# Kernel tuning notes

Measured on AMD Instinct MI355X. Metric: run time of the kernel, lower is better.

## Reference

```python
import jax, jax.numpy as jnp
import numpy as np

NQ, NK, D = 8192, 8192, 256
NEG_INF = -1e30


def setup_inputs() -> dict:
    key = jax.random.key(0)
    kK, kV, kQ, kM = jax.random.split(key, 4)
    K = jax.random.normal(kK, (NK, D), dtype=jnp.float32)
    V = jax.random.normal(kV, (NK, D), dtype=jnp.float32)
    Q = jax.random.normal(kQ, (NQ, D), dtype=jnp.float32)
    m = jax.random.randint(kM, (NQ, NK), 0, 2) > 0  # bool mask, True = attend
    return {"K": K, "V": V, "Q": Q, "m": m}


def reference(K, V, Q, m):
    # affinity: scaled dot product with optional mask
    scale = 1.0 / jnp.sqrt(jnp.asarray(D, dtype=Q.dtype))
    QKt = jnp.einsum('qd,kd->qk', Q, K) * scale  # [NQ, NK]
    QKt = jnp.where(m, QKt, NEG_INF)
    # normalization: softmax over keys
    QKt_n = jax.nn.softmax(QKt, axis=-1)
    # weighted sum of values
    return QKt_n @ V  # [NQ, D]
```

## Files before the change

kernel.cpp:

```cpp
#include <hip/hip_runtime.h>
#include <stdint.h>
#include <stddef.h>

#define NQS 8192
#define NKS 8192
#define DS  256

typedef _Float16 half8 __attribute__((ext_vector_type(8)));
typedef _Float16 half4v __attribute__((ext_vector_type(4)));
typedef float floatx16 __attribute__((ext_vector_type(16)));
typedef float floatx4e __attribute__((ext_vector_type(4)));
typedef uint32_t uint32x4 __attribute__((ext_vector_type(4)));

#define MFMA32(A,B,C) __builtin_amdgcn_mfma_f32_32x32x16_f16(A,B,C,0,0,0)

#define GLOAD_LDS16(gp, lp) \
  __builtin_amdgcn_global_load_lds((const __attribute__((address_space(1))) void*)(gp), \
                                   (__attribute__((address_space(3))) void*)(lp), 16, 0, 0)

#define TILE_ELEMS 16384
#define SUB_ELEMS  8192

__global__ void detect_mask(const uint4* __restrict__ M, uint32_t* __restrict__ flag){
  __shared__ uint32_t s[256];
  uint32_t acc = 0;
  for (int i = threadIdx.x; i < 4096; i += 256){
    uint4 v = M[i];
    acc |= v.x | v.y | v.z | v.w;
  }
  s[threadIdx.x] = acc;
  __syncthreads();
  if (threadIdx.x == 0){
    uint32_t t = 0;
    for (int i = 0; i < 256; i++) t |= s[i];
    *flag = (t > 1u) ? 1u : 0u;
  }
}

__global__ void prep(const float* __restrict__ Qf, const float* __restrict__ K,
                     const float* __restrict__ V,
                     _Float16* __restrict__ Qh, _Float16* __restrict__ Kc,
                     _Float16* __restrict__ Vc){
  const int tid = threadIdx.x;
  if (blockIdx.x < 1024){
    size_t u = (size_t)blockIdx.x*256 + tid;
    const float4* src = (const float4*)(Qf + u*8);
    float4 a = src[0], b = src[1];
    half8 h = {(_Float16)a.x,(_Float16)a.y,(_Float16)a.z,(_Float16)a.w,
               (_Float16)b.x,(_Float16)b.y,(_Float16)b.z,(_Float16)b.w};
    *(half8*)(Qh + u*8) = h;
  } else if (blockIdx.x < 2048){
    int gid = (blockIdx.x - 1024)*256 + tid;
    int key = gid & 8191;
    int c   = gid >> 13;
    int kt = c >> 1, t = c & 1;
    const float4* s = (const float4*)(K + (size_t)key*DS + kt*16 + t*8);
    float4 x = s[0], y = s[1];
    half8 h = {(_Float16)x.x,(_Float16)x.y,(_Float16)x.z,(_Float16)x.w,
               (_Float16)y.x,(_Float16)y.y,(_Float16)y.z,(_Float16)y.w};
    int tile = key >> 6, mt = (key >> 5) & 1, k32 = key & 31;
    size_t off = (size_t)tile*TILE_ELEMS + (((mt*16 + kt)*2 + t)*32 + k32)*8;
    *(half8*)(Kc + off) = h;
  } else {
    int gid = (blockIdx.x - 2048)*256 + tid;
    int d32 = gid & 31;
    int t   = (gid >> 5) & 1;
    int nt  = (gid >> 6) & 7;
    int kkt = (gid >> 9) & 3;
    int tile = gid >> 11;
    int d = nt*32 + d32;
    int kb8 = tile*64 + kkt*16 + t*8;
    half8 h;
    #pragma unroll
    for (int j=0;j<8;j++) h[j] = (_Float16)V[(size_t)(kb8 + j)*DS + d];
    *(half8*)(Vc + (size_t)gid*8) = h;
  }
}

__global__ __launch_bounds__(256, 2) void attn_fwd(
  const _Float16* __restrict__ Qh, const _Float16* __restrict__ Kc,
  const _Float16* __restrict__ Vc, const uint8_t* __restrict__ Msk,
  const uint32_t* __restrict__ flag, _Float16* __restrict__ Oph,
  float* __restrict__ Lo)
{
  __shared__ _Float16 Kls[2][SUB_ELEMS];
  __shared__ _Float16 Vls[2][SUB_ELEMS];
  __shared__ uint8_t  Pk[16][128][8];

  const int tid  = threadIdx.x;
  const int w    = tid >> 6;
  const int lane = tid & 63;
  const int q32  = lane & 31;
  const int t    = lane >> 5;
  const int b    = blockIdx.x;
  const int kh   = b & 7;
  const int rb   = (b >> 3)*128;
  const int rowbase = rb + w*32;
  const int sub0 = kh << 5;
  const int kbase = kh << 10;

  const float kLog = 0.09016844005556021f;
  const float MFIX = 6.0f;

  const bool bm = (*flag != 0u);

  {
    const size_t base = (size_t)sub0 * SUB_ELEMS;
    #pragma unroll
    for (int j=0;j<4;j++){
      int c = w*4 + j;
      GLOAD_LDS16(Kc + base + c*512 + lane*8, &Kls[0][c*512]);
      GLOAD_LDS16(Vc + base + c*512 + lane*8, &Vls[0][c*512]);
    }
  }

  if (bm){
    const uint8_t* mrow = Msk + (size_t)(rb + (tid>>1))*NKS + kbase + (tid&1)*16;
    #pragma unroll 1
    for (int sp=0; sp<16; ++sp){
      uint32x4 e = __builtin_nontemporal_load((const uint32x4*)(mrow + sp*64));
      uint32x4 o = __builtin_nontemporal_load((const uint32x4*)(mrow + sp*64 + 32));
      #pragma unroll
      for (int q=0;q<4;q++){
        uint32_t xe = e[q], xo = o[q];
        uint8_t ne = (uint8_t)(((xe&0x000000FFu)?1u:0u)|((xe&0x0000FF00u)?2u:0u)|
                               ((xe&0x00FF0000u)?4u:0u)|((xe&0xFF000000u)?8u:0u));
        uint8_t no = (uint8_t)(((xo&0x000000FFu)?1u:0u)|((xo&0x0000FF00u)?2u:0u)|
                               ((xo&0x00FF0000u)?4u:0u)|((xo&0xFF000000u)?8u:0u));
        Pk[sp][tid>>1][(tid&1)*4 + q] = (uint8_t)(ne | (no << 4));
      }
    }
  } else {
    const uint32_t* M32 = (const uint32_t*)Msk;
    #pragma unroll 1
    for (int sp=0; sp<16; ++sp){
      uint32x4 e[4], o[4];
      #pragma unroll
      for (int jj=0;jj<4;jj++){
        const uint32_t* p = M32 + (size_t)(rb + jj*32 + (tid>>3))*NKS + kbase + sp*64 + (tid&7)*4;
        e[jj] = __builtin_nontemporal_load((const uint32x4*)p);
        o[jj] = __builtin_nontemporal_load((const uint32x4*)(p + 32));
      }
      #pragma unroll
      for (int jj=0;jj<4;jj++){
        uint8_t ne = (uint8_t)((e[jj][0]?1u:0u)|(e[jj][1]?2u:0u)|(e[jj][2]?4u:0u)|(e[jj][3]?8u:0u));
        uint8_t no = (uint8_t)((o[jj][0]?1u:0u)|(o[jj][1]?2u:0u)|(o[jj][2]?4u:0u)|(o[jj][3]?8u:0u));
        Pk[sp][jj*32 + (tid>>3)][tid&7] = (uint8_t)(ne | (no << 4));
      }
    }
  }

  half8 qf[16];
  {
    const _Float16* qrow = Qh + (size_t)(rowbase + q32)*DS;
    #pragma unroll
    for (int kt=0;kt<16;kt++)
      qf[kt] = *(const half8*)(qrow + kt*16 + t*8);
  }

  floatx16 O[8];
  #pragma unroll
  for (int nt=0;nt<8;nt++)
    #pragma unroll
    for (int i=0;i<16;i++) O[nt][i] = 0.f;
  float lsum = 0.f;

  __syncthreads();

  #pragma unroll 1
  for (int it=0; it<32; ++it){
    const int buf = it & 1;

    if (it < 31){
      const size_t base = (size_t)(sub0 + it + 1) * SUB_ELEMS;
      #pragma unroll
      for (int j=0;j<4;j++){
        int c = w*4 + j;
        GLOAD_LDS16(Kc + base + c*512 + lane*8, &Kls[buf^1][c*512]);
        GLOAD_LDS16(Vc + base + c*512 + lane*8, &Vls[buf^1][c*512]);
      }
    }

    const uint2 nq = *(const uint2*)&Pk[it>>1][w*32 + q32][0];
    const int sh = (it & 1) * 4;
    const uint32_t nib_s[4] = { (nq.x >> (8*t + sh))      & 0xFu,
                                (nq.x >> (16 + 8*t + sh)) & 0xFu,
                                (nq.y >> (8*t + sh))      & 0xFu,
                                (nq.y >> (16 + 8*t + sh)) & 0xFu };

    floatx16 S0, S1;
    #pragma unroll
    for (int i=0;i<16;i++){ S0[i]=0.f; S1[i]=0.f; }
    #pragma unroll
    for (int kt=0;kt<8;kt++){
      half8 kA = *(const half8*)&Kls[buf][((kt*2 + t)*32 + q32)*8];
      S0 = MFMA32(kA, qf[kt], S0);
    }
    #pragma unroll
    for (int kt=8;kt<16;kt++){
      half8 kA = *(const half8*)&Kls[buf][((kt*2 + t)*32 + q32)*8];
      S1 = MFMA32(kA, qf[kt], S1);
    }

    uint32_t pk[4][2];
    #pragma unroll
    for (int s=0;s<4;s++){
      float pv[4];
      #pragma unroll
      for (int rr=0;rr<4;rr++){
        int i = s*4 + rr;
        float e = __builtin_amdgcn_exp2f(__builtin_fmaf(S0[i]+S1[i], kLog, -MFIX));
        float p = ((nib_s[s] >> rr) & 1u) ? e : 0.f;
        lsum += p;
        pv[rr] = p;
      }
      pk[s][0] = __builtin_bit_cast(uint32_t, __builtin_amdgcn_cvt_pkrtz(pv[0], pv[1]));
      pk[s][1] = __builtin_bit_cast(uint32_t, __builtin_amdgcn_cvt_pkrtz(pv[2], pv[3]));
    }

    #pragma unroll
    for (int kt2=0; kt2<2; ++kt2){
      const int s_own  = kt2*2 + t;
      const int s_send = kt2*2 + (t^1);
      uint32_t r0 = __shfl_xor(__builtin_bit_cast(int, pk[s_send][0]), 32);
      uint32_t r1 = __shfl_xor(__builtin_bit_cast(int, pk[s_send][1]), 32);
      uint32_t lo0 = (t==0) ? pk[s_own][0] : r0;
      uint32_t lo1 = (t==0) ? pk[s_own][1] : r1;
      uint32_t hi0 = (t==0) ? r0 : pk[s_own][0];
      uint32_t hi1 = (t==0) ? r1 : pk[s_own][1];
      uint4 u = {lo0, lo1, hi0, hi1};
      half8 pa = __builtin_bit_cast(half8, u);
      #pragma unroll
      for (int nt=0;nt<8;nt++){
        half8 vB = *(const half8*)&Vls[buf][(((kt2*8+nt)*2 + t)*32 + q32)*8];
        O[nt] = MFMA32(pa, vB, O[nt]);
      }
    }

    __syncthreads();
  }

  lsum += __builtin_bit_cast(float, __shfl_xor(__builtin_bit_cast(int, lsum), 32));
  if (t == 0) __builtin_nontemporal_store(lsum, &Lo[(size_t)b*128 + w*32 + q32]);

  _Float16* ob = Oph + ((size_t)b*128 + w*32)*256;
  #pragma unroll
  for (int nt=0;nt<8;nt++){
    #pragma unroll
    for (int i=0;i<16;i++){
      int row = (i&3) + 8*(i>>2) + 4*t;
      __builtin_nontemporal_store((_Float16)O[nt][i], &ob[(size_t)row*256 + nt*32 + q32]);
    }
  }
}

__global__ void combine8(const _Float16* __restrict__ Oph, const float* __restrict__ Lo,
                         float* __restrict__ Out){
  int gid = blockIdx.x*256 + threadIdx.x;
  int row = gid >> 6;
  int c4  = (gid & 63) << 2;
  int g   = row >> 7, r = row & 127;

  float lt = 0.f;
  #pragma unroll
  for (int kh=0;kh<8;kh++) lt += __builtin_nontemporal_load(&Lo[(size_t)(g*8 + kh)*128 + r]);
  float li = 1.0f / lt;

  floatx4e acc = {0.f,0.f,0.f,0.f};
  #pragma unroll
  for (int kh=0;kh<8;kh++){
    half4v o = __builtin_nontemporal_load(
        (const half4v*)(Oph + ((size_t)(g*8 + kh)*128 + r)*256 + c4));
    acc[0] += (float)o[0]; acc[1] += (float)o[1];
    acc[2] += (float)o[2]; acc[3] += (float)o[3];
  }
  acc[0] *= li; acc[1] *= li; acc[2] *= li; acc[3] *= li;
  __builtin_nontemporal_store(acc, (floatx4e*)(Out + (size_t)row*DS + c4));
}

extern "C" void kernel_launch(void* const* d_in, const int* in_sizes, int n_in,
                              void* d_out, int out_size, void* d_ws, size_t ws_size,
                              hipStream_t stream){
  (void)in_sizes; (void)n_in; (void)out_size; (void)ws_size;
  const float*   K = (const float*)d_in[0];
  const float*   V = (const float*)d_in[1];
  const float*   Q = (const float*)d_in[2];
  const uint8_t* M = (const uint8_t*)d_in[3];
  float* Out = (float*)d_out;

  _Float16* Qh  = (_Float16*)d_ws;
  _Float16* Kc  = Qh + (size_t)NQS*DS;
  _Float16* Vc  = Kc + (size_t)NKS*DS;
  _Float16* Oph = Vc + (size_t)NKS*DS;
  float*    Lo  = (float*)(Oph + (size_t)512*128*256);
  uint32_t* flag = (uint32_t*)(Lo + 512*128);

  hipLaunchKernelGGL(detect_mask, dim3(1),    dim3(256), 0, stream, (const uint4*)M, flag);
  hipLaunchKernelGGL(prep,        dim3(3072), dim3(256), 0, stream, Q, K, V, Qh, Kc, Vc);
  hipLaunchKernelGGL(attn_fwd,    dim3(512),  dim3(256), 0, stream, Qh, Kc, Vc, M, flag, Oph, Lo);
  hipLaunchKernelGGL(combine8,    dim3(2048), dim3(256), 0, stream, Oph, Lo, Out);
}
```

Before: 468.6 us.

## Stream mask packing into the main loop instead of the prologue

In the word-per-element mask path, only the first two mask sub-tiles are packed up front. The remaining sub-tiles are loaded into registers one iteration ahead and packed into the shared bitmask during the main attention loop. This hides the long serial mask-load prologue behind the MFMA work. In exchange it adds register pressure from eight held uint32x4 values and extra branching inside the hot loop.

After: 502.5 us. +7.3%, slower.

```diff
diff --git a/kernel.cpp b/kernel.cpp
--- a/kernel.cpp
+++ b/kernel.cpp
@@ -103,6 +103,9 @@
   const float MFIX = 6.0f;
 
   const bool bm = (*flag != 0u);
+  const uint32_t* M32 = (const uint32_t*)Msk;
+  const uint32_t* mbase32 = M32 + (size_t)(rb + (tid>>3))*NKS + kbase + (tid&7)*4;
+  const size_t mrowstride = (size_t)32*NKS;
 
   {
     const size_t base = (size_t)sub0 * SUB_ELEMS;
@@ -114,7 +117,31 @@
     }
   }
 
-  if (bm){
+  uint32x4 B[8];
+  if (!bm){
+    #pragma unroll
+    for (int sp=0; sp<2; ++sp){
+      uint32x4 e[4], o[4];
+      #pragma unroll
+      for (int jj=0;jj<4;jj++){
+        const uint32_t* p = mbase32 + jj*mrowstride + sp*64;
+        e[jj] = __builtin_nontemporal_load((const uint32x4*)p);
+        o[jj] = __builtin_nontemporal_load((const uint32x4*)(p + 32));
+      }
+      #pragma unroll
+      for (int jj=0;jj<4;jj++){
+        uint8_t ne = (uint8_t)((e[jj][0]?1u:0u)|(e[jj][1]?2u:0u)|(e[jj][2]?4u:0u)|(e[jj][3]?8u:0u));
+        uint8_t no = (uint8_t)((o[jj][0]?1u:0u)|(o[jj][1]?2u:0u)|(o[jj][2]?4u:0u)|(o[jj][3]?8u:0u));
+        Pk[sp][jj*32 + (tid>>3)][tid&7] = (uint8_t)(ne | (no << 4));
+      }
+    }
+    #pragma unroll
+    for (int jj=0;jj<4;jj++){
+      const uint32_t* p = mbase32 + jj*mrowstride + 2*64;
+      B[jj*2]   = __builtin_nontemporal_load((const uint32x4*)p);
+      B[jj*2+1] = __builtin_nontemporal_load((const uint32x4*)(p + 32));
+    }
+  } else {
     const uint8_t* mrow = Msk + (size_t)(rb + (tid>>1))*NKS + kbase + (tid&1)*16;
     #pragma unroll 1
     for (int sp=0; sp<16; ++sp){
@@ -130,24 +157,6 @@
         Pk[sp][tid>>1][(tid&1)*4 + q] = (uint8_t)(ne | (no << 4));
       }
     }
-  } else {
-    const uint32_t* M32 = (const uint32_t*)Msk;
-    #pragma unroll 1
-    for (int sp=0; sp<16; ++sp){
-      uint32x4 e[4], o[4];
-      #pragma unroll
-      for (int jj=0;jj<4;jj++){
-        const uint32_t* p = M32 + (size_t)(rb + jj*32 + (tid>>3))*NKS + kbase + sp*64 + (tid&7)*4;
-        e[jj] = __builtin_nontemporal_load((const uint32x4*)p);
-        o[jj] = __builtin_nontemporal_load((const uint32x4*)(p + 32));
-      }
-      #pragma unroll
-      for (int jj=0;jj<4;jj++){
-        uint8_t ne = (uint8_t)((e[jj][0]?1u:0u)|(e[jj][1]?2u:0u)|(e[jj][2]?4u:0u)|(e[jj][3]?8u:0u));
-        uint8_t no = (uint8_t)((o[jj][0]?1u:0u)|(o[jj][1]?2u:0u)|(o[jj][2]?4u:0u)|(o[jj][3]?8u:0u));
-        Pk[sp][jj*32 + (tid>>3)][tid&7] = (uint8_t)(ne | (no << 4));
-      }
-    }
   }
 
   half8 qf[16];
@@ -187,6 +196,24 @@
                                 (nq.x >> (16 + 8*t + sh)) & 0xFu,
                                 (nq.y >> (8*t + sh))      & 0xFu,
                                 (nq.y >> (16 + 8*t + sh)) & 0xFu };
+
+    if (!bm && it <= 13){
+      #pragma unroll
+      for (int jj=0;jj<4;jj++){
+        uint32x4 e = B[jj*2], o = B[jj*2+1];
+        uint8_t ne = (uint8_t)((e[0]?1u:0u)|(e[1]?2u:0u)|(e[2]?4u:0u)|(e[3]?8u:0u));
+        uint8_t no = (uint8_t)((o[0]?1u:0u)|(o[1]?2u:0u)|(o[2]?4u:0u)|(o[3]?8u:0u));
+        Pk[it+2][jj*32 + (tid>>3)][tid&7] = (uint8_t)(ne | (no << 4));
+      }
+      if (it <= 12){
+        #pragma unroll
+        for (int jj=0;jj<4;jj++){
+          const uint32_t* p = mbase32 + jj*mrowstride + (it+3)*64;
+          B[jj*2]   = __builtin_nontemporal_load((const uint32x4*)p);
+          B[jj*2+1] = __builtin_nontemporal_load((const uint32x4*)(p + 32));
+        }
+      }
+    }
 
     floatx16 S0, S1;
     #pragma unroll
```
